# Optimization experiments

Measured on AMD Instinct MI355X. Metric: run time of the kernel, lower is better.

Reference implementation:

```python
import jax, jax.numpy as jnp
import numpy as np

# per-position segment id for seq_len=16: slices [0:1],[1:6],[6:9],[9:10],[10:16]
SEG = np.array([0] + [1]*5 + [2]*3 + [3] + [4]*6, dtype=np.int32)
HEAD_DIM = 3
NUM_HEADS = 2


def setup_inputs() -> dict:
    key = jax.random.key(0)
    ks = jax.random.split(key, 9)
    B = 262144
    s = 1.0 / np.sqrt(6.0)  # torch Linear init scale
    return {
        "x": jax.random.normal(ks[0], (B, 16, 6), dtype=jnp.float32),
        "Wq": jax.random.uniform(ks[1], (5, 6, 6), jnp.float32, -s, s),
        "bq": jax.random.uniform(ks[2], (5, 6), jnp.float32, -s, s),
        "Wk": jax.random.uniform(ks[3], (5, 6, 6), jnp.float32, -s, s),
        "bk": jax.random.uniform(ks[4], (5, 6), jnp.float32, -s, s),
        "Wv": jax.random.uniform(ks[5], (5, 6, 6), jnp.float32, -s, s),
        "bv": jax.random.uniform(ks[6], (5, 6), jnp.float32, -s, s),
        "Wo": jax.random.uniform(ks[7], (6, 6), jnp.float32, -s, s),
        "bo": jax.random.uniform(ks[8], (6,), jnp.float32, -s, s),
    }


def reference(x, Wq, bq, Wk, bk, Wv, bv, Wo, bo):
    B, S, D = x.shape  # S=16, D=6
    seg = jnp.asarray(SEG)

    def seg_proj(W, b):
        # torch Linear: y = x @ W.T + b; gather per-position segment weights
        return jnp.einsum('bsd,sod->bso', x, W[seg]) + b[seg]

    def heads(t):
        return t.reshape(B, S, NUM_HEADS, HEAD_DIM).transpose(0, 2, 1, 3)

    Q = heads(seg_proj(Wq, bq))  # [B,H,S,hd]
    K = heads(seg_proj(Wk, bk))
    V = heads(seg_proj(Wv, bv))

    scores = jnp.einsum('bhqd,bhkd->bhqk', Q, K) / jnp.sqrt(jnp.float32(HEAD_DIM))
    attn = jax.nn.softmax(scores, axis=-1)
    ctx = jnp.einsum('bhqk,bhkd->bhqd', attn, V)
    ctx = ctx.transpose(0, 2, 1, 3).reshape(B, S, D)
    return ctx @ Wo.T + bo
```

## Files before the change

kernel.cpp:

```cpp
#include <hip/hip_runtime.h>

#define QSCALE 0.83294038f

__global__ __launch_bounds__(256)
__attribute__((amdgpu_waves_per_eu(2, 2)))
void attn_seg_kernel(
    const float* __restrict__ x,
    const float* __restrict__ Wq, const float* __restrict__ bq,
    const float* __restrict__ Wk, const float* __restrict__ bk,
    const float* __restrict__ Wv, const float* __restrict__ bv,
    const float* __restrict__ Wo, const float* __restrict__ bo,
    float* __restrict__ out, int nelems)
{
    const int e = blockIdx.x * 256 + threadIdx.x;
    if (e >= nelems) return;

    const float* __restrict__ xe = x + (size_t)e * 96;
    float* __restrict__ oe = out + (size_t)e * 96;

    float K[16][6], V[16][6];

    #pragma unroll
    for (int p = 0; p < 8; ++p) {
        float4 A = *(const float4*)(xe + p * 12);
        float4 B = *(const float4*)(xe + p * 12 + 4);
        float4 C = *(const float4*)(xe + p * 12 + 8);
        float xr[2][6] = {{A.x, A.y, A.z, A.w, B.x, B.y},
                          {B.z, B.w, C.x, C.y, C.z, C.w}};
        #pragma unroll
        for (int h = 0; h < 2; ++h) {
            const int s = p * 2 + h;
            const int sg = (s == 0) ? 0 : (s < 6) ? 1 : (s < 9) ? 2 : (s == 9) ? 3 : 4;
            const float* wk = Wk + sg * 36;
            const float* wv = Wv + sg * 36;
            #pragma unroll
            for (int j = 0; j < 6; ++j) {
                float aK = bk[sg * 6 + j];
                float aV = bv[sg * 6 + j];
                #pragma unroll
                for (int d = 0; d < 6; ++d) {
                    aK += xr[h][d] * wk[j * 6 + d];
                    aV += xr[h][d] * wv[j * 6 + d];
                }
                K[s][j] = aK;
                V[s][j] = aV;
            }
        }
    }

    const float* xq = xe;
    asm volatile("" : "+v"(xq));

    #pragma unroll 1
    for (int p = 0; p < 8; ++p) {
        float4 A = *(const float4*)(xq + p * 12);
        float4 B = *(const float4*)(xq + p * 12 + 4);
        float4 C = *(const float4*)(xq + p * 12 + 8);
        float xr[2][6] = {{A.x, A.y, A.z, A.w, B.x, B.y},
                          {B.z, B.w, C.x, C.y, C.z, C.w}};
        float o2[12];
        #pragma unroll
        for (int h = 0; h < 2; ++h) {
            const int s = p * 2 + h;
            const int sg = (s == 0) ? 0 : (s < 6) ? 1 : (s < 9) ? 2 : (s == 9) ? 3 : 4;
            const float* wq = Wq + sg * 36;

            float q[6];
            #pragma unroll
            for (int j = 0; j < 6; ++j) {
                float a = bq[sg * 6 + j];
                #pragma unroll
                for (int d = 0; d < 6; ++d) a += xr[h][d] * wq[j * 6 + d];
                q[j] = a * QSCALE;
            }

            float s0 = 0.f, s1 = 0.f;
            float c0=0.f,c1=0.f,c2=0.f,c3=0.f,c4=0.f,c5=0.f;
            #pragma unroll
            for (int k = 0; k < 16; ++k) {
                float e0 = __builtin_amdgcn_exp2f(q[0]*K[k][0] + q[1]*K[k][1] + q[2]*K[k][2]);
                float e1 = __builtin_amdgcn_exp2f(q[3]*K[k][3] + q[4]*K[k][4] + q[5]*K[k][5]);
                s0 += e0; s1 += e1;
                c0 += e0*V[k][0]; c1 += e0*V[k][1]; c2 += e0*V[k][2];
                c3 += e1*V[k][3]; c4 += e1*V[k][4]; c5 += e1*V[k][5];
            }
            const float i0 = __builtin_amdgcn_rcpf(s0);
            const float i1 = __builtin_amdgcn_rcpf(s1);
            c0 *= i0; c1 *= i0; c2 *= i0;
            c3 *= i1; c4 *= i1; c5 *= i1;

            #pragma unroll
            for (int i = 0; i < 6; ++i) {
                o2[h*6+i] = bo[i] + c0*Wo[i*6+0] + c1*Wo[i*6+1] + c2*Wo[i*6+2]
                                  + c3*Wo[i*6+3] + c4*Wo[i*6+4] + c5*Wo[i*6+5];
            }
        }
        *(float4*)(oe + p * 12)     = make_float4(o2[0], o2[1], o2[2],  o2[3]);
        *(float4*)(oe + p * 12 + 4) = make_float4(o2[4], o2[5], o2[6],  o2[7]);
        *(float4*)(oe + p * 12 + 8) = make_float4(o2[8], o2[9], o2[10], o2[11]);
    }
}

extern "C" void kernel_launch(void* const* d_in, const int* in_sizes, int n_in,
                              void* d_out, int out_size, void* d_ws, size_t ws_size,
                              hipStream_t stream) {
    const float* x  = (const float*)d_in[0];
    const float* Wq = (const float*)d_in[1];
    const float* bq = (const float*)d_in[2];
    const float* Wk = (const float*)d_in[3];
    const float* bk = (const float*)d_in[4];
    const float* Wv = (const float*)d_in[5];
    const float* bv = (const float*)d_in[6];
    const float* Wo = (const float*)d_in[7];
    const float* bo = (const float*)d_in[8];
    float* out = (float*)d_out;

    const int nelems = in_sizes[0] / 96;
    const int grid   = (nelems + 255) / 256;
    attn_seg_kernel<<<grid, 256, 0, stream>>>(x, Wq, bq, Wk, bk, Wv, bv, Wo, bo, out, nelems);
}
```

Baseline: 265.7 us.

## Split each batch element across four threads by head and key half

New measurement: 309.0 us. +16.3%, slower.

```diff
diff --git a/kernel.cpp b/kernel.cpp
--- a/kernel.cpp
+++ b/kernel.cpp
@@ -2,9 +2,11 @@
 
 #define QSCALE 0.83294038f
 
-__global__ __launch_bounds__(256)
-__attribute__((amdgpu_waves_per_eu(2, 2)))
-void attn_seg_kernel(
+__device__ __forceinline__ int seg_of(int s) {
+    return (s == 0) ? 0 : (s < 6) ? 1 : (s < 9) ? 2 : (s == 9) ? 3 : 4;
+}
+
+__global__ __launch_bounds__(256) void attn_seg_kernel(
     const float* __restrict__ x,
     const float* __restrict__ Wq, const float* __restrict__ bq,
     const float* __restrict__ Wk, const float* __restrict__ bk,
@@ -12,92 +14,121 @@
     const float* __restrict__ Wo, const float* __restrict__ bo,
     float* __restrict__ out, int nelems)
 {
-    const int e = blockIdx.x * 256 + threadIdx.x;
+    const int T = blockIdx.x * 256 + threadIdx.x;
+    const int e = T >> 2;
     if (e >= nelems) return;
+    const int h  = T & 1;
+    const int kh = (T >> 1) & 1;
+    const int kbase = kh << 3;
+    const int hw = h * 18;
+    const int hb = h * 3;
 
     const float* __restrict__ xe = x + (size_t)e * 96;
     float* __restrict__ oe = out + (size_t)e * 96;
 
-    float K[16][6], V[16][6];
+    float K[8][3], V[8][3];
+    float wk[18], wv[18], bk3[3], bv3[3];
+    #pragma unroll
+    for (int si = 0; si < 8; ++si) {
+        if (si == 0 || si == 1 || si == 2 || si == 6) {
+            const int sg = seg_of(kbase + si);
+            const float* wkp = Wk + sg * 36 + hw;
+            const float* wvp = Wv + sg * 36 + hw;
+            #pragma unroll
+            for (int i = 0; i < 9; ++i) {
+                float2 a = *(const float2*)(wkp + 2 * i);
+                wk[2*i] = a.x; wk[2*i+1] = a.y;
+                float2 b = *(const float2*)(wvp + 2 * i);
+                wv[2*i] = b.x; wv[2*i+1] = b.y;
+            }
+            const float* bkp = bk + sg * 6 + hb;
+            const float* bvp = bv + sg * 6 + hb;
+            bk3[0]=bkp[0]; bk3[1]=bkp[1]; bk3[2]=bkp[2];
+            bv3[0]=bvp[0]; bv3[1]=bvp[1]; bv3[2]=bvp[2];
+        }
+        const float* xr = xe + (kbase + si) * 6;
+        float2 a = *(const float2*)(xr);
+        float2 b = *(const float2*)(xr + 2);
+        float2 c = *(const float2*)(xr + 4);
+        #pragma unroll
+        for (int j = 0; j < 3; ++j) {
+            K[si][j] = bk3[j] + a.x*wk[j*6+0] + a.y*wk[j*6+1] + b.x*wk[j*6+2]
+                              + b.y*wk[j*6+3] + c.x*wk[j*6+4] + c.y*wk[j*6+5];
+            V[si][j] = bv3[j] + a.x*wv[j*6+0] + a.y*wv[j*6+1] + b.x*wv[j*6+2]
+                              + b.y*wv[j*6+3] + c.x*wv[j*6+4] + c.y*wv[j*6+5];
+        }
+    }
 
-    #pragma unroll
-    for (int p = 0; p < 8; ++p) {
-        float4 A = *(const float4*)(xe + p * 12);
-        float4 B = *(const float4*)(xe + p * 12 + 4);
-        float4 C = *(const float4*)(xe + p * 12 + 8);
-        float xr[2][6] = {{A.x, A.y, A.z, A.w, B.x, B.y},
-                          {B.z, B.w, C.x, C.y, C.z, C.w}};
+    float wo_own[9], wo_oth[9], bo3[3];
+    {
+        const int ob = 3 - hb;
         #pragma unroll
-        for (int h = 0; h < 2; ++h) {
-            const int s = p * 2 + h;
-            const int sg = (s == 0) ? 0 : (s < 6) ? 1 : (s < 9) ? 2 : (s == 9) ? 3 : 4;
-            const float* wk = Wk + sg * 36;
-            const float* wv = Wv + sg * 36;
-            #pragma unroll
-            for (int j = 0; j < 6; ++j) {
-                float aK = bk[sg * 6 + j];
-                float aV = bv[sg * 6 + j];
-                #pragma unroll
-                for (int d = 0; d < 6; ++d) {
-                    aK += xr[h][d] * wk[j * 6 + d];
-                    aV += xr[h][d] * wv[j * 6 + d];
-                }
-                K[s][j] = aK;
-                V[s][j] = aV;
-            }
+        for (int i = 0; i < 3; ++i) {
+            const float* wr = Wo + (hb + i) * 6;
+            wo_own[i*3+0] = wr[hb+0]; wo_own[i*3+1] = wr[hb+1]; wo_own[i*3+2] = wr[hb+2];
+            wo_oth[i*3+0] = wr[ob+0]; wo_oth[i*3+1] = wr[ob+1]; wo_oth[i*3+2] = wr[ob+2];
+            bo3[i] = bo[hb + i];
         }
     }
 
     const float* xq = xe;
     asm volatile("" : "+v"(xq));
 
-    #pragma unroll 1
-    for (int p = 0; p < 8; ++p) {
-        float4 A = *(const float4*)(xq + p * 12);
-        float4 B = *(const float4*)(xq + p * 12 + 4);
-        float4 C = *(const float4*)(xq + p * 12 + 8);
-        float xr[2][6] = {{A.x, A.y, A.z, A.w, B.x, B.y},
-                          {B.z, B.w, C.x, C.y, C.z, C.w}};
-        float o2[12];
+    #pragma unroll 2
+    for (int q = 0; q < 16; ++q) {
+        const int sg = seg_of(q);
+        const float* wqp = Wq + sg * 36 + hw;
+        float wq[18];
         #pragma unroll
-        for (int h = 0; h < 2; ++h) {
-            const int s = p * 2 + h;
-            const int sg = (s == 0) ? 0 : (s < 6) ? 1 : (s < 9) ? 2 : (s == 9) ? 3 : 4;
-            const float* wq = Wq + sg * 36;
+        for (int i = 0; i < 9; ++i) {
+            float2 a = *(const float2*)(wqp + 2 * i);
+            wq[2*i] = a.x; wq[2*i+1] = a.y;
+        }
+        const float* bqp = bq + sg * 6 + hb;
+        const float qb0 = bqp[0], qb1 = bqp[1], qb2 = bqp[2];
 
-            float q[6];
-            #pragma unroll
-            for (int j = 0; j < 6; ++j) {
-                float a = bq[sg * 6 + j];
-                #pragma unroll
-                for (int d = 0; d < 6; ++d) a += xr[h][d] * wq[j * 6 + d];
-                q[j] = a * QSCALE;
-            }
+        const float* xr = xq + q * 6;
+        float2 a = *(const float2*)(xr);
+        float2 b = *(const float2*)(xr + 2);
+        float2 c = *(const float2*)(xr + 4);
 
-            float s0 = 0.f, s1 = 0.f;
-            float c0=0.f,c1=0.f,c2=0.f,c3=0.f,c4=0.f,c5=0.f;
-            #pragma unroll
-            for (int k = 0; k < 16; ++k) {
-                float e0 = __builtin_amdgcn_exp2f(q[0]*K[k][0] + q[1]*K[k][1] + q[2]*K[k][2]);
-                float e1 = __builtin_amdgcn_exp2f(q[3]*K[k][3] + q[4]*K[k][4] + q[5]*K[k][5]);
-                s0 += e0; s1 += e1;
-                c0 += e0*V[k][0]; c1 += e0*V[k][1]; c2 += e0*V[k][2];
-                c3 += e1*V[k][3]; c4 += e1*V[k][4]; c5 += e1*V[k][5];
-            }
-            const float i0 = __builtin_amdgcn_rcpf(s0);
-            const float i1 = __builtin_amdgcn_rcpf(s1);
-            c0 *= i0; c1 *= i0; c2 *= i0;
-            c3 *= i1; c4 *= i1; c5 *= i1;
+        const float q0 = (qb0 + a.x*wq[0]  + a.y*wq[1]  + b.x*wq[2]
+                              + b.y*wq[3]  + c.x*wq[4]  + c.y*wq[5])  * QSCALE;
+        const float q1 = (qb1 + a.x*wq[6]  + a.y*wq[7]  + b.x*wq[8]
+                              + b.y*wq[9]  + c.x*wq[10] + c.y*wq[11]) * QSCALE;
+        const float q2 = (qb2 + a.x*wq[12] + a.y*wq[13] + b.x*wq[14]
+                              + b.y*wq[15] + c.x*wq[16] + c.y*wq[17]) * QSCALE;
 
-            #pragma unroll
-            for (int i = 0; i < 6; ++i) {
-                o2[h*6+i] = bo[i] + c0*Wo[i*6+0] + c1*Wo[i*6+1] + c2*Wo[i*6+2]
-                                  + c3*Wo[i*6+3] + c4*Wo[i*6+4] + c5*Wo[i*6+5];
-            }
+        float ss = 0.f, c0 = 0.f, c1 = 0.f, c2 = 0.f;
+        #pragma unroll
+        for (int k = 0; k < 8; ++k) {
+            float ee = __builtin_amdgcn_exp2f(q0*K[k][0] + q1*K[k][1] + q2*K[k][2]);
+            ss += ee;
+            c0 += ee*V[k][0]; c1 += ee*V[k][1]; c2 += ee*V[k][2];
         }
-        *(float4*)(oe + p * 12)     = make_float4(o2[0], o2[1], o2[2],  o2[3]);
-        *(float4*)(oe + p * 12 + 4) = make_float4(o2[4], o2[5], o2[6],  o2[7]);
-        *(float4*)(oe + p * 12 + 8) = make_float4(o2[8], o2[9], o2[10], o2[11]);
+
+        ss += __shfl_xor(ss, 2);
+        c0 += __shfl_xor(c0, 2);
+        c1 += __shfl_xor(c1, 2);
+        c2 += __shfl_xor(c2, 2);
+        const float inv = __builtin_amdgcn_rcpf(ss);
+        c0 *= inv; c1 *= inv; c2 *= inv;
+
+        const float d0 = __shfl_xor(c0, 1);
+        const float d1 = __shfl_xor(c1, 1);
+        const float d2 = __shfl_xor(c2, 1);
+
+        const float o0 = bo3[0] + c0*wo_own[0] + c1*wo_own[1] + c2*wo_own[2]
+                                + d0*wo_oth[0] + d1*wo_oth[1] + d2*wo_oth[2];
+        const float o1 = bo3[1] + c0*wo_own[3] + c1*wo_own[4] + c2*wo_own[5]
+                                + d0*wo_oth[3] + d1*wo_oth[4] + d2*wo_oth[5];
+        const float o2 = bo3[2] + c0*wo_own[6] + c1*wo_own[7] + c2*wo_own[8]
+                                + d0*wo_oth[6] + d1*wo_oth[7] + d2*wo_oth[8];
+
+        if (((q >> 3) & 1) == kh) {
+            float* op = oe + q * 6 + hb;
+            op[0] = o0; op[1] = o1; op[2] = o2;
+        }
     }
 }
 
@@ -115,7 +146,8 @@
     const float* bo = (const float*)d_in[8];
     float* out = (float*)d_out;
 
-    const int nelems = in_sizes[0] / 96;
-    const int grid   = (nelems + 255) / 256;
+    const int nelems  = in_sizes[0] / 96;
+    const int nthread = nelems * 4;
+    const int grid    = (nthread + 255) / 256;
     attn_seg_kernel<<<grid, 256, 0, stream>>>(x, Wq, bq, Wk, bk, Wv, bv, Wo, bo, out, nelems);
 }
```

## Split each batch element across 16 wavefronts with K/V shared through LDS

Applied to the files above, without the earlier changes.

Result: faster. 215.9 us (-18.7%).

```diff
diff --git a/kernel.cpp b/kernel.cpp
--- a/kernel.cpp
+++ b/kernel.cpp
@@ -2,9 +2,17 @@
 
 #define QSCALE 0.83294038f
 
-__global__ __launch_bounds__(256)
-__attribute__((amdgpu_waves_per_eu(2, 2)))
-void attn_seg_kernel(
+#define KV_STRIDE 194
+#define OUT_STRIDE 97
+#define KV_FLOATS (64 * KV_STRIDE)
+#define OUT_OFF   KV_FLOATS
+#define LDS_FLOATS (KV_FLOATS + 64 * OUT_STRIDE)
+
+__device__ __forceinline__ int seg_of(int s) {
+    return (s == 0) ? 0 : (s < 6) ? 1 : (s < 9) ? 2 : (s == 9) ? 3 : 4;
+}
+
+__global__ __launch_bounds__(1024) void attn_seg_kernel(
     const float* __restrict__ x,
     const float* __restrict__ Wq, const float* __restrict__ bq,
     const float* __restrict__ Wk, const float* __restrict__ bk,
@@ -12,92 +20,102 @@
     const float* __restrict__ Wo, const float* __restrict__ bo,
     float* __restrict__ out, int nelems)
 {
-    const int e = blockIdx.x * 256 + threadIdx.x;
-    if (e >= nelems) return;
+    __shared__ __align__(16) float lds[LDS_FLOATS];
+    const int t = threadIdx.x;
+    const int e = t & 63;
+    const int s = __builtin_amdgcn_readfirstlane(t >> 6);
+    const int seg = seg_of(s);
+    const int ebase = (int)blockIdx.x << 6;
+    const int eg = ebase + e;
+    const bool valid = eg < nelems;
 
-    const float* __restrict__ xe = x + (size_t)e * 96;
-    float* __restrict__ oe = out + (size_t)e * 96;
+    float x0=0.f,x1=0.f,x2=0.f,x3=0.f,x4=0.f,x5=0.f;
+    if (valid) {
+        const float* xp = x + (size_t)eg * 96 + s * 6;
+        float2 a = *(const float2*)(xp);
+        float2 b = *(const float2*)(xp + 2);
+        float2 c = *(const float2*)(xp + 4);
+        x0=a.x; x1=a.y; x2=b.x; x3=b.y; x4=c.x; x5=c.y;
+    }
 
-    float K[16][6], V[16][6];
+    const float* wk = Wk + seg * 36;
+    const float* wv = Wv + seg * 36;
+    const float* bkp = bk + seg * 6;
+    const float* bvp = bv + seg * 6;
+    float kk[6], vv[6];
+    #pragma unroll
+    for (int j = 0; j < 6; ++j) {
+        kk[j] = bkp[j] + x0*wk[j*6+0] + x1*wk[j*6+1] + x2*wk[j*6+2]
+                       + x3*wk[j*6+3] + x4*wk[j*6+4] + x5*wk[j*6+5];
+        vv[j] = bvp[j] + x0*wv[j*6+0] + x1*wv[j*6+1] + x2*wv[j*6+2]
+                       + x3*wv[j*6+3] + x4*wv[j*6+4] + x5*wv[j*6+5];
+    }
 
+    {
+        float* kv = &lds[e * KV_STRIDE + s * 12];
+        *(float2*)(kv + 0)  = make_float2(kk[0], kk[1]);
+        *(float2*)(kv + 2)  = make_float2(kk[2], kk[3]);
+        *(float2*)(kv + 4)  = make_float2(kk[4], kk[5]);
+        *(float2*)(kv + 6)  = make_float2(vv[0], vv[1]);
+        *(float2*)(kv + 8)  = make_float2(vv[2], vv[3]);
+        *(float2*)(kv + 10) = make_float2(vv[4], vv[5]);
+    }
+
+    const float* wq = Wq + seg * 36;
+    const float* bqp = bq + seg * 6;
+    float q[6];
     #pragma unroll
-    for (int p = 0; p < 8; ++p) {
-        float4 A = *(const float4*)(xe + p * 12);
-        float4 B = *(const float4*)(xe + p * 12 + 4);
-        float4 C = *(const float4*)(xe + p * 12 + 8);
-        float xr[2][6] = {{A.x, A.y, A.z, A.w, B.x, B.y},
-                          {B.z, B.w, C.x, C.y, C.z, C.w}};
+    for (int j = 0; j < 6; ++j) {
+        q[j] = (bqp[j] + x0*wq[j*6+0] + x1*wq[j*6+1] + x2*wq[j*6+2]
+                       + x3*wq[j*6+3] + x4*wq[j*6+4] + x5*wq[j*6+5]) * QSCALE;
+    }
+
+    __syncthreads();
+
+    const float* kvb = &lds[e * KV_STRIDE];
+    float s0 = 0.f, s1 = 0.f;
+    float c0=0.f,c1=0.f,c2=0.f,c3=0.f,c4=0.f,c5=0.f;
+    #pragma unroll
+    for (int k = 0; k < 16; ++k) {
+        float2 ka = *(const float2*)(kvb + k*12 + 0);
+        float2 kb = *(const float2*)(kvb + k*12 + 2);
+        float2 kc = *(const float2*)(kvb + k*12 + 4);
+        float e0 = __builtin_amdgcn_exp2f(q[0]*ka.x + q[1]*ka.y + q[2]*kb.x);
+        float e1 = __builtin_amdgcn_exp2f(q[3]*kb.y + q[4]*kc.x + q[5]*kc.y);
+        float2 va = *(const float2*)(kvb + k*12 + 6);
+        float2 vb = *(const float2*)(kvb + k*12 + 8);
+        float2 vc = *(const float2*)(kvb + k*12 + 10);
+        s0 += e0; s1 += e1;
+        c0 += e0*va.x; c1 += e0*va.y; c2 += e0*vb.x;
+        c3 += e1*vb.y; c4 += e1*vc.x; c5 += e1*vc.y;
+    }
+    const float i0 = __builtin_amdgcn_rcpf(s0);
+    const float i1 = __builtin_amdgcn_rcpf(s1);
+    c0 *= i0; c1 *= i0; c2 *= i0;
+    c3 *= i1; c4 *= i1; c5 *= i1;
+
+    {
+        float* ol = &lds[OUT_OFF + e * OUT_STRIDE + s * 6];
         #pragma unroll
-        for (int h = 0; h < 2; ++h) {
-            const int s = p * 2 + h;
-            const int sg = (s == 0) ? 0 : (s < 6) ? 1 : (s < 9) ? 2 : (s == 9) ? 3 : 4;
-            const float* wk = Wk + sg * 36;
-            const float* wv = Wv + sg * 36;
-            #pragma unroll
-            for (int j = 0; j < 6; ++j) {
-                float aK = bk[sg * 6 + j];
-                float aV = bv[sg * 6 + j];
-                #pragma unroll
-                for (int d = 0; d < 6; ++d) {
-                    aK += xr[h][d] * wk[j * 6 + d];
-                    aV += xr[h][d] * wv[j * 6 + d];
-                }
-                K[s][j] = aK;
-                V[s][j] = aV;
-            }
+        for (int i = 0; i < 6; ++i) {
+            ol[i] = bo[i] + c0*Wo[i*6+0] + c1*Wo[i*6+1] + c2*Wo[i*6+2]
+                          + c3*Wo[i*6+3] + c4*Wo[i*6+4] + c5*Wo[i*6+5];
         }
     }
 
-    const float* xq = xe;
-    asm volatile("" : "+v"(xq));
+    __syncthreads();
 
-    #pragma unroll 1
-    for (int p = 0; p < 8; ++p) {
-        float4 A = *(const float4*)(xq + p * 12);
-        float4 B = *(const float4*)(xq + p * 12 + 4);
-        float4 C = *(const float4*)(xq + p * 12 + 8);
-        float xr[2][6] = {{A.x, A.y, A.z, A.w, B.x, B.y},
-                          {B.z, B.w, C.x, C.y, C.z, C.w}};
-        float o2[12];
-        #pragma unroll
-        for (int h = 0; h < 2; ++h) {
-            const int s = p * 2 + h;
-            const int sg = (s == 0) ? 0 : (s < 6) ? 1 : (s < 9) ? 2 : (s == 9) ? 3 : 4;
-            const float* wq = Wq + sg * 36;
-
-            float q[6];
-            #pragma unroll
-            for (int j = 0; j < 6; ++j) {
-                float a = bq[sg * 6 + j];
-                #pragma unroll
-                for (int d = 0; d < 6; ++d) a += xr[h][d] * wq[j * 6 + d];
-                q[j] = a * QSCALE;
-            }
-
-            float s0 = 0.f, s1 = 0.f;
-            float c0=0.f,c1=0.f,c2=0.f,c3=0.f,c4=0.f,c5=0.f;
-            #pragma unroll
-            for (int k = 0; k < 16; ++k) {
-                float e0 = __builtin_amdgcn_exp2f(q[0]*K[k][0] + q[1]*K[k][1] + q[2]*K[k][2]);
-                float e1 = __builtin_amdgcn_exp2f(q[3]*K[k][3] + q[4]*K[k][4] + q[5]*K[k][5]);
-                s0 += e0; s1 += e1;
-                c0 += e0*V[k][0]; c1 += e0*V[k][1]; c2 += e0*V[k][2];
-                c3 += e1*V[k][3]; c4 += e1*V[k][4]; c5 += e1*V[k][5];
-            }
-            const float i0 = __builtin_amdgcn_rcpf(s0);
-            const float i1 = __builtin_amdgcn_rcpf(s1);
-            c0 *= i0; c1 *= i0; c2 *= i0;
-            c3 *= i1; c4 *= i1; c5 *= i1;
-
-            #pragma unroll
-            for (int i = 0; i < 6; ++i) {
-                o2[h*6+i] = bo[i] + c0*Wo[i*6+0] + c1*Wo[i*6+1] + c2*Wo[i*6+2]
-                                  + c3*Wo[i*6+3] + c4*Wo[i*6+4] + c5*Wo[i*6+5];
-            }
+    {
+        const float* orow = &lds[OUT_OFF + (t >> 4) * OUT_STRIDE + (t & 15) * 6];
+        if (ebase + (t >> 4) < nelems) {
+            float* op = out + (size_t)ebase * 96 + t * 6;
+            float2 a = make_float2(orow[0], orow[1]);
+            float2 b = make_float2(orow[2], orow[3]);
+            float2 c = make_float2(orow[4], orow[5]);
+            *(float2*)(op)     = a;
+            *(float2*)(op + 2) = b;
+            *(float2*)(op + 4) = c;
         }
-        *(float4*)(oe + p * 12)     = make_float4(o2[0], o2[1], o2[2],  o2[3]);
-        *(float4*)(oe + p * 12 + 4) = make_float4(o2[4], o2[5], o2[6],  o2[7]);
-        *(float4*)(oe + p * 12 + 8) = make_float4(o2[8], o2[9], o2[10], o2[11]);
     }
 }
 
@@ -116,6 +134,6 @@
     float* out = (float*)d_out;
 
     const int nelems = in_sizes[0] / 96;
-    const int grid   = (nelems + 255) / 256;
-    attn_seg_kernel<<<grid, 256, 0, stream>>>(x, Wq, bq, Wk, bk, Wv, bv, Wo, bo, out, nelems);
+    const int grid   = (nelems + 63) / 64;
+    attn_seg_kernel<<<grid, 1024, 0, stream>>>(x, Wq, bq, Wk, bk, Wv, bv, Wo, bo, out, nelems);
 }
```
